# Performance work log

Measured on AMD Instinct MI355X. Metric: run time of the kernel, lower is better.

The kernel has to match this reference:

```python
import jax, jax.numpy as jnp
import numpy as np

N = 100000
IN_DIM = 128
HID = 64
OUT = 4


def _gcn_conv(x, W, b, src, dst, deg_inv_sqrt):
    """PyG GCNConv: linear transform, then symmetric-normalized scatter-add.
    src/dst already include self-loops; deg_inv_sqrt precomputed over them."""
    h = x @ W                                   # [N, H]
    norm = deg_inv_sqrt[src] * deg_inv_sqrt[dst]  # [E+N]
    msg = h[src] * norm[:, None]                # gather + scale, [E+N, H]
    out = jax.ops.segment_sum(msg, dst, num_segments=N)  # scatter-add
    return out + b


def setup_inputs() -> dict:
    key = jax.random.key(0)
    ks = jax.random.split(key, 8)
    E = 1600000
    x = jax.random.normal(ks[0], (N, IN_DIM), dtype=jnp.float32)
    edge_index = jax.random.randint(ks[1], (2, E), 0, N, dtype=jnp.int32)
    # Glorot-ish init for weights
    W1 = jax.random.normal(ks[2], (IN_DIM, HID), dtype=jnp.float32) / np.sqrt(IN_DIM)
    b1 = jnp.zeros((HID,), dtype=jnp.float32)
    W2 = jax.random.normal(ks[3], (HID, HID), dtype=jnp.float32) / np.sqrt(HID)
    b2 = jnp.zeros((HID,), dtype=jnp.float32)
    Wfc = jax.random.normal(ks[4], (HID, OUT), dtype=jnp.float32) / np.sqrt(HID)
    bfc = jnp.zeros((OUT,), dtype=jnp.float32)
    return {"x": x, "edge_index": edge_index, "W1": W1, "b1": b1,
            "W2": W2, "b2": b2, "Wfc": Wfc, "bfc": bfc}


def reference(x, edge_index, W1, b1, W2, b2, Wfc, bfc):
    # Add self-loops (GCNConv default add_self_loops=True)
    loops = jnp.arange(N, dtype=edge_index.dtype)
    src = jnp.concatenate([edge_index[0], loops])
    dst = jnp.concatenate([edge_index[1], loops])
    # Symmetric normalization: deg computed at aggregation targets (dst)
    deg = jax.ops.segment_sum(jnp.ones_like(dst, dtype=x.dtype), dst,
                              num_segments=N)
    deg_inv_sqrt = jnp.where(deg > 0, jax.lax.rsqrt(deg), 0.0)

    h = _gcn_conv(x, W1, b1, src, dst, deg_inv_sqrt)
    h = jax.nn.relu(h)                 # dropout is identity in eval mode
    h = _gcn_conv(h, W2, b2, src, dst, deg_inv_sqrt)
    h = jax.nn.relu(h)
    return h @ Wfc + bfc               # [N, 4]
```

## Files before the change

kernel.cpp:

```cpp
#include <hip/hip_runtime.h>
#include <hip/hip_fp16.h>


#define BCAP 5120
#define BINB 1024
#define CHUNK 1600
#define CAP  64
#define LCAP 32

typedef float v2f __attribute__((ext_vector_type(2)));
typedef _Float16 f16x8 __attribute__((ext_vector_type(8)));
typedef float f32x4 __attribute__((ext_vector_type(4)));

__global__ __launch_bounds__(256) void k_bin_gemm1(
        const int* __restrict__ src, const int* __restrict__ dst, int e,
        int* bcur, unsigned* __restrict__ binned,
        const float* __restrict__ X, const float* __restrict__ W1,
        __half* __restrict__ Hh, int n) {
    __shared__ union {
        struct {
            unsigned ec[CHUNK];
            unsigned short eb[CHUNK];
            int lh[512], lbase[512], lr[512];
        } b;
        struct {
            _Float16 As[64 * 136];
            _Float16 Bs[64 * 136];
        } g;
    } sm;

    int t = threadIdx.x;

    if ((int)blockIdx.x < BINB) {
        auto& B = sm.b;
        for (int i = t; i < 512; i += 256) { B.lh[i] = 0; B.lr[i] = 0; }
        __syncthreads();
        int chunk = (e + BINB - 1) / BINB;
        int lo = blockIdx.x * chunk;
        int hi = min(e, lo + chunk);
        for (int i = lo + t; i < hi; i += 256) {
            int d = dst[i];
            int b = d >> 8;
            B.ec[i - lo] = ((unsigned)src[i] << 8) | (unsigned)(d & 255);
            B.eb[i - lo] = (unsigned short)b;
            atomicAdd(&B.lh[b], 1);
        }
        __syncthreads();
        for (int i = t; i < 512; i += 256)
            B.lbase[i] = B.lh[i] ? atomicAdd(&bcur[i], B.lh[i]) : 0;
        __syncthreads();
        int cnt = hi - lo;
        for (int i = t; i < cnt; i += 256) {
            int b = B.eb[i];
            int r = B.lbase[b] + atomicAdd(&B.lr[b], 1);
            if (r < BCAP)
                binned[(size_t)b * BCAP + r] = B.ec[i];
        }
    } else {
        constexpr int K = 128, KP = 136;
        _Float16* As = sm.g.As;
        _Float16* Bs = sm.g.Bs;
        _Float16* H = (_Float16*)Hh;

        #pragma unroll
        for (int p = 0; p < 8; ++p) {
            int i = t + p * 256;
            int k = i >> 4, nn4 = (i & 15) << 2;
            float4 v = ((const float4*)W1)[i];
            Bs[(nn4 + 0) * KP + k] = (_Float16)v.x;
            Bs[(nn4 + 1) * KP + k] = (_Float16)v.y;
            Bs[(nn4 + 2) * KP + k] = (_Float16)v.z;
            Bs[(nn4 + 3) * KP + k] = (_Float16)v.w;
        }

        int row0 = ((int)blockIdx.x - BINB) * 64;
        #pragma unroll
        for (int p = 0; p < 4; ++p) {
            int gi  = t + p * 256;
            int row = gi >> 4, sg = gi & 15;
            int grow = row0 + row;
            float4 v0 = make_float4(0.f, 0.f, 0.f, 0.f), v1 = v0;
            if (grow < n) {
                v0 = *(const float4*)(X + (size_t)grow * K + sg * 8);
                v1 = *(const float4*)(X + (size_t)grow * K + sg * 8 + 4);
            }
            union { __half2 h[4]; float4 f; } u;
            u.h[0] = __floats2half2_rn(v0.x, v0.y);
            u.h[1] = __floats2half2_rn(v0.z, v0.w);
            u.h[2] = __floats2half2_rn(v1.x, v1.y);
            u.h[3] = __floats2half2_rn(v1.z, v1.w);
            *(float4*)(As + row * KP + sg * 8) = u.f;
        }
        __syncthreads();

        int wv   = t >> 6;
        int lane = t & 63;
        int m    = lane & 15;
        int quad = lane >> 4;
        int r0   = wv * 16;

        f32x4 acc[4] = {};
        #pragma unroll
        for (int kb = 0; kb < K / 32; ++kb) {
            f16x8 af = *(const f16x8*)(As + (r0 + m) * KP + quad * 8 + kb * 32);
            #pragma unroll
            for (int nt = 0; nt < 4; ++nt) {
                f16x8 bf = *(const f16x8*)(Bs + (nt * 16 + m) * KP + quad * 8 + kb * 32);
                acc[nt] = __builtin_amdgcn_mfma_f32_16x16x32_f16(af, bf, acc[nt], 0, 0, 0);
            }
        }

        int gr[4];
        #pragma unroll
        for (int r = 0; r < 4; ++r)
            gr[r] = row0 + r0 + quad * 4 + r;
        #pragma unroll
        for (int nt = 0; nt < 4; ++nt)
            #pragma unroll
            for (int r = 0; r < 4; ++r) {
                if (gr[r] < n)
                    H[(size_t)gr[r] * 64 + nt * 16 + m] = (_Float16)acc[nt][r];
                else if (gr[r] == n)
                    H[(size_t)n * 64 + nt * 16 + m] = (_Float16)0.f;
            }
    }
}

__global__ __launch_bounds__(256) void k_bucket2(const unsigned* __restrict__ binned,
                                                 const int* __restrict__ bcur,
                                                 int n, int* __restrict__ cnt,
                                                 int* __restrict__ slots) {
    __shared__ int lists[256 * (LCAP + 1)];
    __shared__ int lcnt[256];
    int b = blockIdx.x, t = threadIdx.x;
    int node0 = b << 8;
    size_t ebase = (size_t)b * BCAP;
    int ecnt = min(bcur[b], BCAP);
    lcnt[t] = 0;
    __syncthreads();
    for (int j = t; j < ecnt; j += 256) {
        unsigned ed = binned[ebase + j];
        int ld = ed & 255u;
        int s  = (int)(ed >> 8);
        int r  = atomicAdd(&lcnt[ld], 1);
        if (r < LCAP)
            lists[ld * (LCAP + 1) + r] = s;
        else if (r < CAP)
            slots[((size_t)(node0 + ld) << 6) + r] = s;
    }
    __syncthreads();
    if (node0 + t < n) cnt[node0 + t] = lcnt[t];
    for (int k = t; k < 256 * LCAP; k += 256) {
        int ld = k >> 5;
        int r  = k & (LCAP - 1);
        if (r < min(lcnt[ld], LCAP) && node0 + ld < n)
            slots[((size_t)(node0 + ld) << 6) + r] =
                lists[ld * (LCAP + 1) + r];
    }
}

__global__ __launch_bounds__(256) void k_gemm2(const __half* __restrict__ X,
                                               const float* __restrict__ W2,
                                               const int* __restrict__ cnt,
                                               __half* __restrict__ Hh, int n) {
    constexpr int K = 64, KP = 72;
    __shared__ _Float16 As[64 * KP];
    __shared__ _Float16 Bs[64 * KP];

    int t = threadIdx.x;
    _Float16* H = (_Float16*)Hh;

    #pragma unroll
    for (int p = 0; p < 4; ++p) {
        int i = t + p * 256;
        int k = i >> 4, nn4 = (i & 15) << 2;
        float4 v = ((const float4*)W2)[i];
        Bs[(nn4 + 0) * KP + k] = (_Float16)v.x;
        Bs[(nn4 + 1) * KP + k] = (_Float16)v.y;
        Bs[(nn4 + 2) * KP + k] = (_Float16)v.z;
        Bs[(nn4 + 3) * KP + k] = (_Float16)v.w;
    }

    int row0 = blockIdx.x * 64;
    const __half* Xh = X;
    #pragma unroll
    for (int p = 0; p < 2; ++p) {
        int gi  = t + p * 256;
        int row = gi >> 3, sg = gi & 7;
        int grow = row0 + row;
        float4 v = make_float4(0.f, 0.f, 0.f, 0.f);
        if (grow < n)
            v = *(const float4*)(Xh + (size_t)grow * K + sg * 8);
        *(float4*)(As + row * KP + sg * 8) = v;
    }
    __syncthreads();

    int wv   = t >> 6;
    int lane = t & 63;
    int m    = lane & 15;
    int quad = lane >> 4;
    int r0   = wv * 16;

    f32x4 acc[4] = {};
    #pragma unroll
    for (int kb = 0; kb < K / 32; ++kb) {
        f16x8 af = *(const f16x8*)(As + (r0 + m) * KP + quad * 8 + kb * 32);
        #pragma unroll
        for (int nt = 0; nt < 4; ++nt) {
            f16x8 bf = *(const f16x8*)(Bs + (nt * 16 + m) * KP + quad * 8 + kb * 32);
            acc[nt] = __builtin_amdgcn_mfma_f32_16x16x32_f16(af, bf, acc[nt], 0, 0, 0);
        }
    }

    float dv[4]; int gr[4];
    #pragma unroll
    for (int r = 0; r < 4; ++r) {
        gr[r] = row0 + r0 + quad * 4 + r;
        dv[r] = (gr[r] < n) ? rsqrtf((float)(cnt[gr[r]] + 1)) : 0.f;
    }
    #pragma unroll
    for (int nt = 0; nt < 4; ++nt)
        #pragma unroll
        for (int r = 0; r < 4; ++r) {
            if (gr[r] < n)
                H[(size_t)gr[r] * 64 + nt * 16 + m] =
                    (_Float16)(acc[nt][r] * dv[r]);
            else if (gr[r] == n)
                H[(size_t)n * 64 + nt * 16 + m] = (_Float16)0.f;
        }
}

__device__ inline void add_row(const __half* __restrict__ hp, int s, int c4,
                               v2f& lo, v2f& hi) {
    float2 raw = *(const float2*)(hp + (size_t)s * 64 + c4);
    const __half2* p = (const __half2*)&raw;
    float2 l = __half22float2(p[0]);
    float2 h = __half22float2(p[1]);
    lo += (v2f){ l.x, l.y };
    hi += (v2f){ h.x, h.y };
}

__device__ inline void fma_row(const __half* __restrict__ hp, int s, int c4,
                               float w, v2f& lo, v2f& hi) {
    float2 raw = *(const float2*)(hp + (size_t)s * 64 + c4);
    const __half2* p = (const __half2*)&raw;
    float2 l = __half22float2(p[0]);
    float2 h = __half22float2(p[1]);
    lo += w * (v2f){ l.x, l.y };
    hi += w * (v2f){ h.x, h.y };
}

template<bool FUSE, bool SCALE>
__global__ __launch_bounds__(256) void k_gather(const __half* __restrict__ hp,
                                                const int* __restrict__ slots,
                                                const int* __restrict__ cnt,
                                                const float* __restrict__ bias,
                                                void* __restrict__ outb,
                                                const float* __restrict__ Wfc,
                                                const float* __restrict__ bfc,
                                                int n) {
    int lane = threadIdx.x & 63;
    int wid  = (blockIdx.x * blockDim.x + threadIdx.x) >> 6;
    if (wid >= n) return;
    int d    = wid;
    int esub = lane >> 4;
    int c4   = (lane & 15) * 4;

    size_t start = (size_t)d << 6;
    int num = cnt[d];
    int lim = min(num, CAP);
    int idx = (lane < lim) ? slots[start + lane] : 0;
    float dsv = 0.f;
    if constexpr (SCALE)
        dsv = rsqrtf((float)(cnt[idx] + 1));
    float dd = rsqrtf((float)(num + 1));

    v2f aL[4] = {}, aH[4] = {};
    if (esub == 0) {
        if constexpr (SCALE) fma_row(hp, d, c4, dd, aL[0], aH[0]);
        else                 add_row(hp, d, c4, aL[0], aH[0]);
    }

    int j = 0;
    for (; j + 16 <= lim; j += 16) {
        int s0 = __shfl(idx, j + esub);
        int s1 = __shfl(idx, j + 4 + esub);
        int s2 = __shfl(idx, j + 8 + esub);
        int s3 = __shfl(idx, j + 12 + esub);
        if constexpr (SCALE) {
            float w0 = __shfl(dsv, j + esub);
            float w1 = __shfl(dsv, j + 4 + esub);
            float w2 = __shfl(dsv, j + 8 + esub);
            float w3 = __shfl(dsv, j + 12 + esub);
            fma_row(hp, s0, c4, w0, aL[0], aH[0]);
            fma_row(hp, s1, c4, w1, aL[1], aH[1]);
            fma_row(hp, s2, c4, w2, aL[2], aH[2]);
            fma_row(hp, s3, c4, w3, aL[3], aH[3]);
        } else {
            add_row(hp, s0, c4, aL[0], aH[0]);
            add_row(hp, s1, c4, aL[1], aH[1]);
            add_row(hp, s2, c4, aL[2], aH[2]);
            add_row(hp, s3, c4, aL[3], aH[3]);
        }
    }
    for (; j < lim; j += 4) {
        int jj = j + esub;
        int sr = __shfl(idx, jj);
        int s  = (jj < lim) ? sr : n;
        if constexpr (SCALE) {
            float w = __shfl(dsv, jj);
            fma_row(hp, s, c4, w, aL[0], aH[0]);
        } else {
            add_row(hp, s, c4, aL[0], aH[0]);
        }
    }
    v2f sL = (aL[0] + aL[1]) + (aL[2] + aL[3]);
    v2f sH = (aH[0] + aH[1]) + (aH[2] + aH[3]);
    float4 a0 = make_float4(sL.x, sL.y, sH.x, sH.y);
    #pragma unroll
    for (int o = 16; o <= 32; o <<= 1) {
        a0.x += __shfl_xor(a0.x, o);
        a0.y += __shfl_xor(a0.y, o);
        a0.z += __shfl_xor(a0.z, o);
        a0.w += __shfl_xor(a0.w, o);
    }
    float4 bb = *(const float4*)(bias + c4);
    float4 o;
    o.x = fmaxf(bb.x + dd * a0.x, 0.f);
    o.y = fmaxf(bb.y + dd * a0.y, 0.f);
    o.z = fmaxf(bb.z + dd * a0.z, 0.f);
    o.w = fmaxf(bb.w + dd * a0.w, 0.f);
    if (!FUSE) {
        if (esub == 0) {
            union { __half2 h[2]; float2 f; } u;
            u.h[0] = __floats2half2_rn(o.x, o.y);
            u.h[1] = __floats2half2_rn(o.z, o.w);
            *(float2*)((__half*)outb + (size_t)d * 64 + c4) = u.f;
        }
    } else {
        const float4* W4 = (const float4*)Wfc;
        float4 w0 = W4[c4 + 0], w1 = W4[c4 + 1], w2 = W4[c4 + 2], w3 = W4[c4 + 3];
        float4 p;
        p.x = o.x * w0.x + o.y * w1.x + o.z * w2.x + o.w * w3.x;
        p.y = o.x * w0.y + o.y * w1.y + o.z * w2.y + o.w * w3.y;
        p.z = o.x * w0.z + o.y * w1.z + o.z * w2.z + o.w * w3.z;
        p.w = o.x * w0.w + o.y * w1.w + o.z * w2.w + o.w * w3.w;
        #pragma unroll
        for (int q = 1; q <= 8; q <<= 1) {
            p.x += __shfl_xor(p.x, q);
            p.y += __shfl_xor(p.y, q);
            p.z += __shfl_xor(p.z, q);
            p.w += __shfl_xor(p.w, q);
        }
        if (lane == 0) {
            float4 bf = *(const float4*)bfc;
            float4 r = make_float4(p.x + bf.x, p.y + bf.y, p.z + bf.z, p.w + bf.w);
            ((float4*)outb)[d] = r;
        }
    }
}

static inline size_t align256(size_t x) { return (x + 255) & ~(size_t)255; }

extern "C" void kernel_launch(void* const* d_in, const int* in_sizes, int n_in,
                              void* d_out, int out_size, void* d_ws, size_t ws_size,
                              hipStream_t stream) {
    const float* x   = (const float*)d_in[0];
    const int*   ei  = (const int*)d_in[1];
    const float* W1  = (const float*)d_in[2];
    const float* b1  = (const float*)d_in[3];
    const float* W2  = (const float*)d_in[4];
    const float* b2  = (const float*)d_in[5];
    const float* Wfc = (const float*)d_in[6];
    const float* bfc = (const float*)d_in[7];
    float* out = (float*)d_out;

    int n = in_sizes[0] / 128;
    int e = in_sizes[1] / 2;
    const int* src = ei;
    const int* dst = ei + e;

    char* ws = (char*)d_ws;
    size_t p = 0;
    int*      cnt    = (int*)     (ws + p); p = align256(p + (size_t)n * 4);
    int*      bcur   = (int*)     (ws + p); p = align256(p + 512 * 4);
    unsigned* binned = (unsigned*)(ws + p); p = align256(p + (size_t)512 * BCAP * 4);
    int*      slots  = (int*)     (ws + p); p = align256(p + (size_t)n * CAP * 4);
    __half*   hbuf   = (__half*)  (ws + p); p = align256(p + (size_t)(n + 1) * 64 * 2);
    __half*   a1h    = (__half*)  (ws + p);

    int gb  = (n + 64) / 64;
    int nbk = (n + 255) / 256;

    hipMemsetAsync(bcur, 0, 512 * sizeof(int), stream);
    k_bin_gemm1<<<BINB + gb, 256, 0, stream>>>(src, dst, e, bcur, binned,
                                               x, W1, hbuf, n);
    k_bucket2<<<nbk, 256, 0, stream>>>(binned, bcur, n, cnt, slots);

    k_gather<false, true><<<(n * 64 + 255) / 256, 256, 0, stream>>>(
        hbuf, slots, cnt, b1, a1h, nullptr, nullptr, n);

    k_gemm2<<<gb, 256, 0, stream>>>(a1h, W2, cnt, hbuf, n);
    k_gather<true, false><<<(n * 64 + 255) / 256, 256, 0, stream>>>(
        hbuf, slots, cnt, b2, out, Wfc, bfc, n);
}
```

Baseline: 265.9 us.

## Load GEMM A fragments directly from global and double rows per block

Both GEMM stages stop staging the input activations through shared memory. Each lane now loads its MFMA A fragment straight from global memory, converting from fp32 to fp16 in registers for the first GEMM. Each wave handles two 16-row M tiles, so a block covers 128 rows and reuses each B fragment for two MFMAs, halving the grid. This removes LDS writes and reads for A and halves the per-block W staging. The cost is strided, less coalesced global loads, and the zero row at index n is only written when n is not a multiple of 128.

```diff
diff --git a/kernel.cpp b/kernel.cpp
--- a/kernel.cpp
+++ b/kernel.cpp
@@ -11,6 +11,15 @@
 typedef float v2f __attribute__((ext_vector_type(2)));
 typedef _Float16 f16x8 __attribute__((ext_vector_type(8)));
 typedef float f32x4 __attribute__((ext_vector_type(4)));
+
+__device__ inline f16x8 cvt8(float4 v0, float4 v1) {
+    union { __half2 h[4]; f16x8 v; } u;
+    u.h[0] = __floats2half2_rn(v0.x, v0.y);
+    u.h[1] = __floats2half2_rn(v0.z, v0.w);
+    u.h[2] = __floats2half2_rn(v1.x, v1.y);
+    u.h[3] = __floats2half2_rn(v1.z, v1.w);
+    return u.v;
+}
 
 __global__ __launch_bounds__(256) void k_bin_gemm1(
         const int* __restrict__ src, const int* __restrict__ dst, int e,
@@ -24,7 +33,6 @@
             int lh[512], lbase[512], lr[512];
         } b;
         struct {
-            _Float16 As[64 * 136];
             _Float16 Bs[64 * 136];
         } g;
     } sm;
@@ -58,7 +66,6 @@
         }
     } else {
         constexpr int K = 128, KP = 136;
-        _Float16* As = sm.g.As;
         _Float16* Bs = sm.g.Bs;
         _Float16* H = (_Float16*)Hh;
 
@@ -72,57 +79,55 @@
             Bs[(nn4 + 2) * KP + k] = (_Float16)v.z;
             Bs[(nn4 + 3) * KP + k] = (_Float16)v.w;
         }
-
-        int row0 = ((int)blockIdx.x - BINB) * 64;
-        #pragma unroll
-        for (int p = 0; p < 4; ++p) {
-            int gi  = t + p * 256;
-            int row = gi >> 4, sg = gi & 15;
-            int grow = row0 + row;
-            float4 v0 = make_float4(0.f, 0.f, 0.f, 0.f), v1 = v0;
-            if (grow < n) {
-                v0 = *(const float4*)(X + (size_t)grow * K + sg * 8);
-                v1 = *(const float4*)(X + (size_t)grow * K + sg * 8 + 4);
-            }
-            union { __half2 h[4]; float4 f; } u;
-            u.h[0] = __floats2half2_rn(v0.x, v0.y);
-            u.h[1] = __floats2half2_rn(v0.z, v0.w);
-            u.h[2] = __floats2half2_rn(v1.x, v1.y);
-            u.h[3] = __floats2half2_rn(v1.z, v1.w);
-            *(float4*)(As + row * KP + sg * 8) = u.f;
-        }
         __syncthreads();
 
         int wv   = t >> 6;
         int lane = t & 63;
         int m    = lane & 15;
         int quad = lane >> 4;
-        int r0   = wv * 16;
-
-        f32x4 acc[4] = {};
+        int row0 = ((int)blockIdx.x - BINB) * 128;
+        int r0   = row0 + wv * 32;
+        int ra   = r0 + m;
+        int rb   = r0 + 16 + m;
+        bool va = ra < n, vb = rb < n;
+        const float* Xa = X + (size_t)ra * K + quad * 8;
+        const float* Xb = X + (size_t)rb * K + quad * 8;
+        const float4 z4 = make_float4(0.f, 0.f, 0.f, 0.f);
+
+        f32x4 acc[2][4] = {};
         #pragma unroll
         for (int kb = 0; kb < K / 32; ++kb) {
-            f16x8 af = *(const f16x8*)(As + (r0 + m) * KP + quad * 8 + kb * 32);
+            float4 a0 = va ? *(const float4*)(Xa + kb * 32)     : z4;
+            float4 a1 = va ? *(const float4*)(Xa + kb * 32 + 4) : z4;
+            float4 b0 = vb ? *(const float4*)(Xb + kb * 32)     : z4;
+            float4 b1 = vb ? *(const float4*)(Xb + kb * 32 + 4) : z4;
+            f16x8 af0 = cvt8(a0, a1);
+            f16x8 af1 = cvt8(b0, b1);
             #pragma unroll
             for (int nt = 0; nt < 4; ++nt) {
                 f16x8 bf = *(const f16x8*)(Bs + (nt * 16 + m) * KP + quad * 8 + kb * 32);
-                acc[nt] = __builtin_amdgcn_mfma_f32_16x16x32_f16(af, bf, acc[nt], 0, 0, 0);
+                acc[0][nt] = __builtin_amdgcn_mfma_f32_16x16x32_f16(af0, bf, acc[0][nt], 0, 0, 0);
+                acc[1][nt] = __builtin_amdgcn_mfma_f32_16x16x32_f16(af1, bf, acc[1][nt], 0, 0, 0);
             }
         }
 
-        int gr[4];
-        #pragma unroll
-        for (int r = 0; r < 4; ++r)
-            gr[r] = row0 + r0 + quad * 4 + r;
-        #pragma unroll
-        for (int nt = 0; nt < 4; ++nt)
+        #pragma unroll
+        for (int mt = 0; mt < 2; ++mt) {
+            int gr[4];
             #pragma unroll
-            for (int r = 0; r < 4; ++r) {
-                if (gr[r] < n)
-                    H[(size_t)gr[r] * 64 + nt * 16 + m] = (_Float16)acc[nt][r];
-                else if (gr[r] == n)
-                    H[(size_t)n * 64 + nt * 16 + m] = (_Float16)0.f;
-            }
+            for (int r = 0; r < 4; ++r)
+                gr[r] = r0 + mt * 16 + quad * 4 + r;
+            #pragma unroll
+            for (int nt = 0; nt < 4; ++nt)
+                #pragma unroll
+                for (int r = 0; r < 4; ++r) {
+                    if (gr[r] < n)
+                        H[(size_t)gr[r] * 64 + nt * 16 + m] =
+                            (_Float16)acc[mt][nt][r];
+                    else if (gr[r] == n)
+                        H[(size_t)n * 64 + nt * 16 + m] = (_Float16)0.f;
+                }
+        }
     }
 }
 
@@ -164,7 +169,6 @@
                                                const int* __restrict__ cnt,
                                                __half* __restrict__ Hh, int n) {
     constexpr int K = 64, KP = 72;
-    __shared__ _Float16 As[64 * KP];
     __shared__ _Float16 Bs[64 * KP];
 
     int t = threadIdx.x;
@@ -180,54 +184,52 @@
         Bs[(nn4 + 2) * KP + k] = (_Float16)v.z;
         Bs[(nn4 + 3) * KP + k] = (_Float16)v.w;
     }
-
-    int row0 = blockIdx.x * 64;
-    const __half* Xh = X;
-    #pragma unroll
-    for (int p = 0; p < 2; ++p) {
-        int gi  = t + p * 256;
-        int row = gi >> 3, sg = gi & 7;
-        int grow = row0 + row;
-        float4 v = make_float4(0.f, 0.f, 0.f, 0.f);
-        if (grow < n)
-            v = *(const float4*)(Xh + (size_t)grow * K + sg * 8);
-        *(float4*)(As + row * KP + sg * 8) = v;
-    }
     __syncthreads();
 
     int wv   = t >> 6;
     int lane = t & 63;
     int m    = lane & 15;
     int quad = lane >> 4;
-    int r0   = wv * 16;
-
-    f32x4 acc[4] = {};
+    int row0 = blockIdx.x * 128;
+    int r0   = row0 + wv * 32;
+    int ra   = r0 + m;
+    int rb   = r0 + 16 + m;
+    bool va = ra < n, vb = rb < n;
+    const _Float16* Xa = (const _Float16*)X + (size_t)ra * K + quad * 8;
+    const _Float16* Xb = (const _Float16*)X + (size_t)rb * K + quad * 8;
+
+    f32x4 acc[2][4] = {};
     #pragma unroll
     for (int kb = 0; kb < K / 32; ++kb) {
-        f16x8 af = *(const f16x8*)(As + (r0 + m) * KP + quad * 8 + kb * 32);
+        f16x8 af0 = va ? *(const f16x8*)(Xa + kb * 32) : (f16x8)0;
+        f16x8 af1 = vb ? *(const f16x8*)(Xb + kb * 32) : (f16x8)0;
         #pragma unroll
         for (int nt = 0; nt < 4; ++nt) {
             f16x8 bf = *(const f16x8*)(Bs + (nt * 16 + m) * KP + quad * 8 + kb * 32);
-            acc[nt] = __builtin_amdgcn_mfma_f32_16x16x32_f16(af, bf, acc[nt], 0, 0, 0);
-        }
-    }
-
-    float dv[4]; int gr[4];
+            acc[0][nt] = __builtin_amdgcn_mfma_f32_16x16x32_f16(af0, bf, acc[0][nt], 0, 0, 0);
+            acc[1][nt] = __builtin_amdgcn_mfma_f32_16x16x32_f16(af1, bf, acc[1][nt], 0, 0, 0);
+        }
+    }
+
     #pragma unroll
-    for (int r = 0; r < 4; ++r) {
-        gr[r] = row0 + r0 + quad * 4 + r;
-        dv[r] = (gr[r] < n) ? rsqrtf((float)(cnt[gr[r]] + 1)) : 0.f;
-    }
-    #pragma unroll
-    for (int nt = 0; nt < 4; ++nt)
+    for (int mt = 0; mt < 2; ++mt) {
+        float dv[4]; int gr[4];
         #pragma unroll
         for (int r = 0; r < 4; ++r) {
-            if (gr[r] < n)
-                H[(size_t)gr[r] * 64 + nt * 16 + m] =
-                    (_Float16)(acc[nt][r] * dv[r]);
-            else if (gr[r] == n)
-                H[(size_t)n * 64 + nt * 16 + m] = (_Float16)0.f;
-        }
+            gr[r] = r0 + mt * 16 + quad * 4 + r;
+            dv[r] = (gr[r] < n) ? rsqrtf((float)(cnt[gr[r]] + 1)) : 0.f;
+        }
+        #pragma unroll
+        for (int nt = 0; nt < 4; ++nt)
+            #pragma unroll
+            for (int r = 0; r < 4; ++r) {
+                if (gr[r] < n)
+                    H[(size_t)gr[r] * 64 + nt * 16 + m] =
+                        (_Float16)(acc[mt][nt][r] * dv[r]);
+                else if (gr[r] == n)
+                    H[(size_t)n * 64 + nt * 16 + m] = (_Float16)0.f;
+            }
+    }
 }
 
 __device__ inline void add_row(const __half* __restrict__ hp, int s, int c4,
@@ -389,7 +391,7 @@
     __half*   hbuf   = (__half*)  (ws + p); p = align256(p + (size_t)(n + 1) * 64 * 2);
     __half*   a1h    = (__half*)  (ws + p);
 
-    int gb  = (n + 64) / 64;
+    int gb  = (n + 127) / 128;
     int nbk = (n + 255) / 256;
 
     hipMemsetAsync(bcur, 0, 512 * sizeof(int), stream);
```

New measurement: 288.6 us. 1.09x slower.
